# Optimization experiments

Hardware: AMD Instinct MI355X
Metric: run time of the kernel (lower is better)

Reference implementation:

```python
import jax, jax.numpy as jnp
import numpy as np

B, H, S, D = 2, 16, 2048, 64
DILATION_RATE = 2

def dilated_global_mask(seq_len: int, dilation_rate: int) -> jnp.ndarray:
    # mask[i, j] = 1 if |i - j| % dilation_rate == 0 else 0  -> [S, S] float32
    i = jnp.arange(seq_len)[:, None]
    j = jnp.arange(seq_len)[None, :]
    return ((jnp.abs(i - j) % dilation_rate) == 0).astype(jnp.float32)

def setup_inputs() -> dict:
    key = jax.random.key(0)
    kq, kk, kv = jax.random.split(key, 3)
    queries = jax.random.normal(kq, (B, H, S, D), dtype=jnp.float32)
    keys = jax.random.normal(kk, (B, H, S, D), dtype=jnp.float32)
    values = jax.random.normal(kv, (B, H, S, D), dtype=jnp.float32)
    return {"queries": queries, "keys": keys, "values": values}

def reference(queries, keys, values):
    depth = queries.shape[-1]
    # scores: [B, H, S, S]
    scores = jnp.einsum("bhqd,bhkd->bhqk", queries, keys)
    scores = scores / jnp.sqrt(jnp.asarray(depth, dtype=jnp.float32))
    gmask = dilated_global_mask(keys.shape[-2], DILATION_RATE)  # [S, S]
    # NOTE: multiplicative masking (masked scores become 0, not -inf), as in source
    masked_scores = scores * gmask
    attention_probs = jax.nn.softmax(masked_scores, axis=-1)
    # dropout is identity at inference (training=None)
    out = jnp.einsum("bhqk,bhkd->bhqd", attention_probs, values)
    return out
```

## Files before the change

kernel.cpp:

```cpp
#include <hip/hip_runtime.h>
#include <hip/hip_bf16.h>


#define B_   2
#define H_   16
#define S_   2048
#define D_   64
#define SP_  1024
#define BQ   128
#define FBQ  64
#define BK   64
#define NKT  (SP_ / BK)

#define QSCALE 0.180336884f

#if __has_builtin(__builtin_amdgcn_exp2f)
#define EXP2(x) __builtin_amdgcn_exp2f(x)
#else
#define EXP2(x) exp2f(x)
#endif

typedef __bf16 bf16x8 __attribute__((ext_vector_type(8)));
typedef __bf16 bf16x4 __attribute__((ext_vector_type(4)));
typedef float  f32x4  __attribute__((ext_vector_type(4)));
typedef short  s16x4  __attribute__((ext_vector_type(4)));

static __device__ __forceinline__ f32x4 mfma16(bf16x4 a, bf16x4 b, f32x4 c) {
    return __builtin_amdgcn_mfma_f32_16x16x16bf16_1k(
        __builtin_bit_cast(s16x4, a), __builtin_bit_cast(s16x4, b), c, 0, 0, 0);
}

#define KSW(r, c8) ((((c8) ^ ((r) & 7)) << 3))

__global__ __launch_bounds__(256) void conv2_kernel(const float* __restrict__ K,
                                                    const float* __restrict__ V,
                                                    __bf16* __restrict__ Kf,
                                                    __bf16* __restrict__ Vt,
                                                    __bf16* __restrict__ vsp) {
    const int id  = blockIdx.x;
    const int l2  = id >> 3;
    const int bh  = (id & 7) * 4 + (l2 & 3);
    const int kt  = l2 >> 2;
    const int tid = threadIdx.x;
    const float* Kb = K + (size_t)bh * S_ * D_;
    const float* Vb = V + (size_t)bh * S_ * D_;

    #pragma unroll
    for (int i = 0; i < 4; ++i) {
        const int u    = tid + 256 * i;
        const int par  = u >> 9;
        const int f    = (u >> 6) & 7;
        const int lane = u & 63;
        const int key  = kt * 64 + (f & 3) * 16 + (lane & 15);
        const int col  = ((f >> 2) * 4 + (lane >> 4)) * 8;
        const float* src = Kb + (size_t)(par + 2 * key) * D_ + col;
        const float4 a = *(const float4*)src;
        const float4 b = *(const float4*)(src + 4);
        bf16x8 w;
        w[0] = (__bf16)a.x; w[1] = (__bf16)a.y;
        w[2] = (__bf16)a.z; w[3] = (__bf16)a.w;
        w[4] = (__bf16)b.x; w[5] = (__bf16)b.y;
        w[6] = (__bf16)b.z; w[7] = (__bf16)b.w;
        const size_t bp = (size_t)(bh * 2 + par);
        *(bf16x8*)&Kf[((bp * NKT + kt) * 8 + f) * 512 + lane * 8] = w;
    }

    __shared__ __align__(16) __bf16 vt[64][80];
    const int row = tid >> 2;
    const int c0  = (tid & 3) * 16;

    #pragma unroll
    for (int par = 0; par < 2; ++par) {
        {
            const float* vsrc = Vb + (size_t)(par + 2 * (kt * 64 + row)) * D_ + c0;
            const float4 a0 = *(const float4*)(vsrc);
            const float4 a1 = *(const float4*)(vsrc + 4);
            const float4 a2 = *(const float4*)(vsrc + 8);
            const float4 a3 = *(const float4*)(vsrc + 12);
            bf16x8 w0, w1;
            w0[0] = (__bf16)a0.x; w0[1] = (__bf16)a0.y;
            w0[2] = (__bf16)a0.z; w0[3] = (__bf16)a0.w;
            w0[4] = (__bf16)a1.x; w0[5] = (__bf16)a1.y;
            w0[6] = (__bf16)a1.z; w0[7] = (__bf16)a1.w;
            w1[0] = (__bf16)a2.x; w1[1] = (__bf16)a2.y;
            w1[2] = (__bf16)a2.z; w1[3] = (__bf16)a2.w;
            w1[4] = (__bf16)a3.x; w1[5] = (__bf16)a3.y;
            w1[6] = (__bf16)a3.z; w1[7] = (__bf16)a3.w;
            *(bf16x8*)&vt[row][c0]     = w0;
            *(bf16x8*)&vt[row][c0 + 8] = w1;
        }
        __syncthreads();
        {
            const int d   = row;
            const int dt  = d >> 4;
            const int l15 = d & 15;
            const size_t bp = (size_t)(bh * 2 + par);
            const size_t tb = (bp * NKT + kt) * 16;
            float vsum = 0.f;
            #pragma unroll
            for (int cc2 = 0; cc2 < 2; ++cc2) {
                const int cc  = (tid & 3) * 2 + cc2;
                const int kt4 = cc >> 1;
                const int qa  = (cc & 1) * 2;
                bf16x4 wa, wb;
                #pragma unroll
                for (int m = 0; m < 4; ++m) {
                    const __bf16 x = vt[cc * 8 + m][d];
                    const __bf16 y = vt[cc * 8 + 4 + m][d];
                    wa[m] = x; wb[m] = y;
                    vsum += (float)x + (float)y;
                }
                const int g = kt4 * 4 + dt;
                *(bf16x4*)&Vt[(tb + g) * 256 + (qa * 16 + l15) * 4]       = wa;
                *(bf16x4*)&Vt[(tb + g) * 256 + ((qa + 1) * 16 + l15) * 4] = wb;
            }
            vsum += __shfl_down(vsum, 1);
            vsum += __shfl_down(vsum, 2);
            if ((tid & 3) == 0)
                vsp[(bp * NKT + kt) * 64 + d] = (__bf16)vsum;
        }
        __syncthreads();
    }
}

__global__ __launch_bounds__(256, 2) void attn6_kernel(const float* __restrict__ Q,
                                                       const __bf16* __restrict__ Kf,
                                                       const __bf16* __restrict__ Vt,
                                                       const __bf16* __restrict__ vsp,
                                                       float* __restrict__ out) {
    const int id  = blockIdx.x;
    const int l2  = id >> 3;
    const int bh  = (id & 7) * 4 + (l2 & 3);
    const int par = (l2 >> 2) & 1;
    const int qt  = l2 >> 3;
    const int bp  = bh * 2 + par;
    const int tid  = threadIdx.x;
    const int lane = tid & 63;
    const int wave = tid >> 6;
    const int l15  = lane & 15;
    const int quad = lane >> 4;

    __shared__ __align__(16) char arena[32768];

    const size_t base = (size_t)bh * S_ * D_;

    bf16x8 qf[2][2];
    #pragma unroll
    for (int qt2 = 0; qt2 < 2; ++qt2) {
        const int qrow = qt * BQ + wave * 32 + qt2 * 16 + l15;
        const float* qsrc = Q + base + (size_t)(par + 2 * qrow) * D_ + quad * 8;
        #pragma unroll
        for (int ks = 0; ks < 2; ++ks) {
            const float4 a = *(const float4*)(qsrc + ks * 32);
            const float4 b = *(const float4*)(qsrc + ks * 32 + 4);
            bf16x8 w;
            w[0] = (__bf16)(a.x * QSCALE); w[1] = (__bf16)(a.y * QSCALE);
            w[2] = (__bf16)(a.z * QSCALE); w[3] = (__bf16)(a.w * QSCALE);
            w[4] = (__bf16)(b.x * QSCALE); w[5] = (__bf16)(b.y * QSCALE);
            w[6] = (__bf16)(b.z * QSCALE); w[7] = (__bf16)(b.w * QSCALE);
            qf[qt2][ks] = w;
        }
    }

    const uint4* Kt4 = (const uint4*)(Kf + (size_t)bp * NKT * 4096);
    const uint4* Vt4 = (const uint4*)(Vt + (size_t)bp * NKT * 4096);
    uint4 sk0, sk1, sv0, sv1;

    auto issue_loads = [&](int kt) {
        const int o = kt * 512 + tid;
        sk0 = Kt4[o]; sk1 = Kt4[o + 256];
        sv0 = Vt4[o]; sv1 = Vt4[o + 256];
    };
    auto stage = [&](int buf) {
        uint4* kd = (uint4*)(arena + buf * 8192);
        uint4* vd = (uint4*)(arena + 16384 + buf * 8192);
        kd[tid] = sk0; kd[tid + 256] = sk1;
        vd[tid] = sv0; vd[tid + 256] = sv1;
    };

    issue_loads(0);
    stage(0);
    __syncthreads();

    f32x4 acc[2][4];
    #pragma unroll
    for (int q2 = 0; q2 < 2; ++q2)
        #pragma unroll
        for (int dt = 0; dt < 4; ++dt) acc[q2][dt] = (f32x4){0.f, 0.f, 0.f, 0.f};
    float l_acc[2] = {0.f, 0.f};

    for (int kt = 0; kt < NKT; ++kt) {
        const int cur = kt & 1;
        const bool pf = (kt + 1 < NKT);

        if (pf) issue_loads(kt + 1);

        const char* kb = arena + cur * 8192;
        const char* vb = arena + 16384 + cur * 8192;

        bf16x8 ka[2][4];
        #pragma unroll
        for (int ks = 0; ks < 2; ++ks)
            #pragma unroll
            for (int kt4 = 0; kt4 < 4; ++kt4)
                ka[ks][kt4] = *(const bf16x8*)(kb + (ks * 4 + kt4) * 1024 + lane * 16);
        bf16x4 va[4][4];
        #pragma unroll
        for (int kt4 = 0; kt4 < 4; ++kt4)
            #pragma unroll
            for (int dt = 0; dt < 4; ++dt)
                va[kt4][dt] = *(const bf16x4*)(vb + (kt4 * 4 + dt) * 512 + lane * 8);

        #pragma unroll
        for (int qt2 = 0; qt2 < 2; ++qt2) {
            f32x4 st[4];
            #pragma unroll
            for (int kt4 = 0; kt4 < 4; ++kt4) st[kt4] = (f32x4){0.f, 0.f, 0.f, 0.f};
            #pragma unroll
            for (int ks = 0; ks < 2; ++ks)
                #pragma unroll
                for (int kt4 = 0; kt4 < 4; ++kt4)
                    st[kt4] = __builtin_amdgcn_mfma_f32_16x16x32_bf16(
                        ka[ks][kt4], qf[qt2][ks], st[kt4], 0, 0, 0);
            #pragma unroll
            for (int kt4 = 0; kt4 < 4; ++kt4) {
                const float p0 = EXP2(st[kt4][0]);
                const float p1 = EXP2(st[kt4][1]);
                const float p2 = EXP2(st[kt4][2]);
                const float p3 = EXP2(st[kt4][3]);
                l_acc[qt2] += (p0 + p1) + (p2 + p3);
                bf16x4 pb;
                pb[0] = (__bf16)p0; pb[1] = (__bf16)p1;
                pb[2] = (__bf16)p2; pb[3] = (__bf16)p3;
                #pragma unroll
                for (int dt = 0; dt < 4; ++dt)
                    acc[qt2][dt] = mfma16(va[kt4][dt], pb, acc[qt2][dt]);
            }
        }

        if (pf) stage(1 - cur);
        __syncthreads();
    }

    float rz[2];
    #pragma unroll
    for (int qt2 = 0; qt2 < 2; ++qt2) {
        float Z = l_acc[qt2];
        Z += __shfl_xor(Z, 16);
        Z += __shfl_xor(Z, 32);
        rz[qt2] = 1.0f / (Z + 1024.0f);
    }
    const __bf16* vsb = vsp + (size_t)(bh * 2 + (1 - par)) * NKT * 64;
    f32x4 vs4[4];
    #pragma unroll
    for (int dt = 0; dt < 4; ++dt) {
        f32x4 s = (f32x4){0.f, 0.f, 0.f, 0.f};
        #pragma unroll
        for (int kt = 0; kt < NKT; ++kt) {
            const bf16x4 v = *(const bf16x4*)&vsb[kt * 64 + dt * 16 + quad * 4];
            s[0] += (float)v[0]; s[1] += (float)v[1];
            s[2] += (float)v[2]; s[3] += (float)v[3];
        }
        vs4[dt] = s;
    }

    float* tw = (float*)arena + wave * (16 * 68);
    #pragma unroll
    for (int qt2 = 0; qt2 < 2; ++qt2) {
        #pragma unroll
        for (int dt = 0; dt < 4; ++dt) {
            const f32x4 o = (acc[qt2][dt] + vs4[dt]) * rz[qt2];
            *(f32x4*)&tw[l15 * 68 + dt * 16 + quad * 4] = o;
        }
        #pragma unroll
        for (int i = 0; i < 4; ++i) {
            const int q = i * 4 + quad;
            const f32x4 ov = *(const f32x4*)&tw[q * 68 + l15 * 4];
            const int qg = par + 2 * (qt * BQ + wave * 32 + qt2 * 16 + q);
            *(f32x4*)&out[base + (size_t)qg * D_ + l15 * 4] = ov;
        }
    }
}

__global__ __launch_bounds__(1024) void vsum_kernel(const float* __restrict__ V,
                                                    float* __restrict__ vs) {
    const int bp  = blockIdx.x;
    const int bh  = bp >> 1;
    const int par = bp & 1;
    const int d   = threadIdx.x & 63;
    const int rg  = threadIdx.x >> 6;
    const float* Vb = V + (size_t)bh * S_ * D_;
    float s = 0.f;
    for (int r = rg; r < SP_; r += 16)
        s += Vb[(size_t)(par + 2 * r) * D_ + d];
    __shared__ float red[16][64];
    red[rg][d] = s;
    __syncthreads();
    if (rg == 0) {
        float t = 0.f;
        #pragma unroll
        for (int i = 0; i < 16; ++i) t += red[i][d];
        vs[(size_t)bp * 64 + d] = t;
    }
}

__global__ __launch_bounds__(256, 4) void attn_fb_kernel(const float* __restrict__ Q,
                                                         const float* __restrict__ K,
                                                         const float* __restrict__ V,
                                                         const float* __restrict__ vs,
                                                         float* __restrict__ out) {
    const int bh  = blockIdx.x;
    const int par = blockIdx.y;
    const int qt  = blockIdx.z;
    const int tid  = threadIdx.x;
    const int lane = tid & 63;
    const int wave = tid >> 6;
    const int l15  = lane & 15;
    const int quad = lane >> 4;

    __shared__ __align__(16) char arena[32768];
    __bf16 (*kbuf)[BK][64] = (__bf16 (*)[BK][64])arena;
    __bf16 (*vbuf)[D_][64] = (__bf16 (*)[D_][64])(arena + 16384);

    const size_t base = (size_t)bh * S_ * D_;
    const float* Qb = Q + base;
    const float* Kb = K + base;
    const float* Vb = V + base;

    bf16x8 qf[2];
    {
        const int qrow = qt * FBQ + wave * 16 + l15;
        const float* qsrc = Qb + (size_t)(par + 2 * qrow) * D_ + quad * 8;
        #pragma unroll
        for (int ks = 0; ks < 2; ++ks) {
            const float4 a = *(const float4*)(qsrc + ks * 32);
            const float4 b = *(const float4*)(qsrc + ks * 32 + 4);
            bf16x8 w;
            w[0] = (__bf16)(a.x * QSCALE); w[1] = (__bf16)(a.y * QSCALE);
            w[2] = (__bf16)(a.z * QSCALE); w[3] = (__bf16)(a.w * QSCALE);
            w[4] = (__bf16)(b.x * QSCALE); w[5] = (__bf16)(b.y * QSCALE);
            w[6] = (__bf16)(b.z * QSCALE); w[7] = (__bf16)(b.w * QSCALE);
            qf[ks] = w;
        }
    }

    const int kr0 = tid >> 3;
    const int kc8 = tid & 7;
    float4 pka[2], pkb[2];
    float  pv[16];

    auto issue_loads = [&](int kt) {
        #pragma unroll
        for (int i = 0; i < 2; ++i) {
            const int r = i * 32 + kr0;
            const float* ksrc = Kb + (size_t)(par + 2 * (kt * BK + r)) * D_ + kc8 * 8;
            pka[i] = *(const float4*)ksrc;
            pkb[i] = *(const float4*)(ksrc + 4);
        }
        #pragma unroll
        for (int i = 0; i < 2; ++i) {
            const int c = wave + 4 * i;
            const float* vsrc = Vb + (size_t)(par + 2 * (kt * BK + c * 8)) * D_ + lane;
            #pragma unroll
            for (int j = 0; j < 8; ++j)
                pv[i * 8 + j] = vsrc[(size_t)(2 * j) * D_];
        }
    };
    auto stage = [&](int buf) {
        #pragma unroll
        for (int i = 0; i < 2; ++i) {
            const int r = i * 32 + kr0;
            bf16x8 w;
            w[0] = (__bf16)pka[i].x; w[1] = (__bf16)pka[i].y;
            w[2] = (__bf16)pka[i].z; w[3] = (__bf16)pka[i].w;
            w[4] = (__bf16)pkb[i].x; w[5] = (__bf16)pkb[i].y;
            w[6] = (__bf16)pkb[i].z; w[7] = (__bf16)pkb[i].w;
            *(bf16x8*)&kbuf[buf][r][KSW(r, kc8)] = w;
        }
        #pragma unroll
        for (int i = 0; i < 2; ++i) {
            const int c = wave + 4 * i;
            bf16x8 w;
            #pragma unroll
            for (int j = 0; j < 8; ++j) w[j] = (__bf16)pv[i * 8 + j];
            *(bf16x8*)&vbuf[buf][lane][KSW(lane, c)] = w;
        }
    };

    issue_loads(0);
    stage(0);
    __syncthreads();

    f32x4 acc[4];
    #pragma unroll
    for (int dt = 0; dt < 4; ++dt) acc[dt] = (f32x4){0.f, 0.f, 0.f, 0.f};
    float l_acc = 0.f;

    for (int kt = 0; kt < NKT; ++kt) {
        const int cur = kt & 1;
        const bool pf = (kt + 1 < NKT);
        if (pf) issue_loads(kt + 1);

        const __bf16 (*kb)[64] = kbuf[cur];
        const __bf16 (*vb)[64] = vbuf[cur];

        bf16x8 ka[2][4];
        #pragma unroll
        for (int ks = 0; ks < 2; ++ks)
            #pragma unroll
            for (int kt4 = 0; kt4 < 4; ++kt4) {
                const int R = kt4 * 16 + l15;
                ka[ks][kt4] = *(const bf16x8*)&kb[R][KSW(R, ks * 4 + quad)];
            }
        bf16x4 va[4][4];
        #pragma unroll
        for (int dt = 0; dt < 4; ++dt) {
            const int R = dt * 16 + l15;
            const int ro = R & 7;
            #pragma unroll
            for (int kt4 = 0; kt4 < 4; ++kt4) {
                const int ch = (kt4 * 2 + (quad >> 1)) ^ ro;
                va[kt4][dt] = *(const bf16x4*)&vb[R][ch * 8 + (quad & 1) * 4];
            }
        }

        f32x4 st[4];
        #pragma unroll
        for (int kt4 = 0; kt4 < 4; ++kt4) st[kt4] = (f32x4){0.f, 0.f, 0.f, 0.f};
        #pragma unroll
        for (int ks = 0; ks < 2; ++ks)
            #pragma unroll
            for (int kt4 = 0; kt4 < 4; ++kt4)
                st[kt4] = __builtin_amdgcn_mfma_f32_16x16x32_bf16(
                    ka[ks][kt4], qf[ks], st[kt4], 0, 0, 0);
        #pragma unroll
        for (int kt4 = 0; kt4 < 4; ++kt4) {
            const float p0 = EXP2(st[kt4][0]);
            const float p1 = EXP2(st[kt4][1]);
            const float p2 = EXP2(st[kt4][2]);
            const float p3 = EXP2(st[kt4][3]);
            l_acc += (p0 + p1) + (p2 + p3);
            bf16x4 pb;
            pb[0] = (__bf16)p0; pb[1] = (__bf16)p1;
            pb[2] = (__bf16)p2; pb[3] = (__bf16)p3;
            #pragma unroll
            for (int dt = 0; dt < 4; ++dt)
                acc[dt] = mfma16(va[kt4][dt], pb, acc[dt]);
        }

        if (pf) stage(1 - cur);
        __syncthreads();
    }

    float Z = l_acc;
    Z += __shfl_xor(Z, 16);
    Z += __shfl_xor(Z, 32);
    const float rz = 1.0f / (Z + 1024.0f);
    const float* vso = vs + ((size_t)(bh * 2 + (1 - par))) * 64;

    float* tw = (float*)arena + wave * (16 * 68);
    #pragma unroll
    for (int dt = 0; dt < 4; ++dt) {
        const f32x4 vs4 = *(const f32x4*)&vso[dt * 16 + quad * 4];
        const f32x4 o = (acc[dt] + vs4) * rz;
        *(f32x4*)&tw[l15 * 68 + dt * 16 + quad * 4] = o;
    }
    #pragma unroll
    for (int i = 0; i < 4; ++i) {
        const int q = i * 4 + quad;
        const f32x4 ov = *(const f32x4*)&tw[q * 68 + l15 * 4];
        const int qg = par + 2 * (qt * FBQ + wave * 16 + q);
        *(f32x4*)&out[base + (size_t)qg * D_ + l15 * 4] = ov;
    }
}

extern "C" void kernel_launch(void* const* d_in, const int* in_sizes, int n_in,
                              void* d_out, int out_size, void* d_ws, size_t ws_size,
                              hipStream_t stream) {
    const float* Q = (const float*)d_in[0];
    const float* K = (const float*)d_in[1];
    const float* V = (const float*)d_in[2];
    float* out = (float*)d_out;

    const size_t KF_BYTES  = (size_t)64 * NKT * 4096 * sizeof(__bf16);
    const size_t VT_BYTES  = (size_t)64 * NKT * 4096 * sizeof(__bf16);
    const size_t VSP_BYTES = (size_t)64 * NKT * 64 * sizeof(__bf16);
    const size_t need = KF_BYTES + VT_BYTES + VSP_BYTES;

    if (ws_size >= need) {
        __bf16* Kf  = (__bf16*)d_ws;
        __bf16* Vt  = (__bf16*)((char*)d_ws + KF_BYTES);
        __bf16* vsp = (__bf16*)((char*)d_ws + KF_BYTES + VT_BYTES);
        conv2_kernel<<<dim3(512), dim3(256), 0, stream>>>(K, V, Kf, Vt, vsp);
        attn6_kernel<<<dim3(512), dim3(256), 0, stream>>>(Q, Kf, Vt, vsp, out);
    } else {
        float* vsn = (float*)d_ws;
        vsum_kernel<<<dim3(B_ * H_ * 2), dim3(1024), 0, stream>>>(V, vsn);
        attn_fb_kernel<<<dim3(B_ * H_, 2, SP_ / FBQ), dim3(256), 0, stream>>>(
            Q, K, V, vsn, out);
    }
}
```

Before: 121.2 us.

## Deepen K/V prefetch to two tiles ahead with barriers that skip vmcnt wait

The main attention loop now keeps two register sets of global K/V loads in flight, so loads are issued two tiles ahead. It also replaces __syncthreads with a custom barrier that waits only on LDS counters and leaves outstanding global loads pending. Together these aim to hide global-memory latency behind the MFMA work. The cost is higher register pressure at two blocks per CU, and correctness now depends on the compiler inserting vmcnt waits before the register values are staged.

```diff
diff --git a/kernel.cpp b/kernel.cpp
--- a/kernel.cpp
+++ b/kernel.cpp
@@ -31,6 +31,15 @@
 }
 
 #define KSW(r, c8) ((((c8) ^ ((r) & 7)) << 3))
+
+#define BARRIER_KEEP_VMCNT()                                   \
+    do {                                                       \
+        __builtin_amdgcn_sched_barrier(0);                     \
+        asm volatile("s_waitcnt lgkmcnt(0)" ::: "memory");     \
+        __builtin_amdgcn_sched_barrier(0);                     \
+        __builtin_amdgcn_s_barrier();                          \
+        __builtin_amdgcn_sched_barrier(0);                     \
+    } while (0)
 
 __global__ __launch_bounds__(256) void conv2_kernel(const float* __restrict__ K,
                                                     const float* __restrict__ V,
@@ -123,7 +132,7 @@
     }
 }
 
-__global__ __launch_bounds__(256, 2) void attn6_kernel(const float* __restrict__ Q,
+__global__ __launch_bounds__(256, 2) void attn7_kernel(const float* __restrict__ Q,
                                                        const __bf16* __restrict__ Kf,
                                                        const __bf16* __restrict__ Vt,
                                                        const __bf16* __restrict__ vsp,
@@ -164,23 +173,31 @@
 
     const uint4* Kt4 = (const uint4*)(Kf + (size_t)bp * NKT * 4096);
     const uint4* Vt4 = (const uint4*)(Vt + (size_t)bp * NKT * 4096);
-    uint4 sk0, sk1, sv0, sv1;
-
-    auto issue_loads = [&](int kt) {
+    uint4 skP0, skP1, svP0, svP1;
+    uint4 skQ0, skQ1, svQ0, svQ1;
+
+    auto issueP = [&](int kt) {
         const int o = kt * 512 + tid;
-        sk0 = Kt4[o]; sk1 = Kt4[o + 256];
-        sv0 = Vt4[o]; sv1 = Vt4[o + 256];
-    };
-    auto stage = [&](int buf) {
+        skP0 = Kt4[o]; skP1 = Kt4[o + 256];
+        svP0 = Vt4[o]; svP1 = Vt4[o + 256];
+    };
+    auto issueQ = [&](int kt) {
+        const int o = kt * 512 + tid;
+        skQ0 = Kt4[o]; skQ1 = Kt4[o + 256];
+        svQ0 = Vt4[o]; svQ1 = Vt4[o + 256];
+    };
+    auto stageP = [&](int buf) {
         uint4* kd = (uint4*)(arena + buf * 8192);
         uint4* vd = (uint4*)(arena + 16384 + buf * 8192);
-        kd[tid] = sk0; kd[tid + 256] = sk1;
-        vd[tid] = sv0; vd[tid + 256] = sv1;
-    };
-
-    issue_loads(0);
-    stage(0);
-    __syncthreads();
+        kd[tid] = skP0; kd[tid + 256] = skP1;
+        vd[tid] = svP0; vd[tid + 256] = svP1;
+    };
+    auto stageQ = [&](int buf) {
+        uint4* kd = (uint4*)(arena + buf * 8192);
+        uint4* vd = (uint4*)(arena + 16384 + buf * 8192);
+        kd[tid] = skQ0; kd[tid + 256] = skQ1;
+        vd[tid] = svQ0; vd[tid + 256] = svQ1;
+    };
 
     f32x4 acc[2][4];
     #pragma unroll
@@ -189,15 +206,7 @@
         for (int dt = 0; dt < 4; ++dt) acc[q2][dt] = (f32x4){0.f, 0.f, 0.f, 0.f};
     float l_acc[2] = {0.f, 0.f};
 
-    for (int kt = 0; kt < NKT; ++kt) {
-        const int cur = kt & 1;
-        const bool pf = (kt + 1 < NKT);
-
-        if (pf) issue_loads(kt + 1);
-
-        const char* kb = arena + cur * 8192;
-        const char* vb = arena + 16384 + cur * 8192;
-
+    auto compute = [&](const char* kb, const char* vb) {
         bf16x8 ka[2][4];
         #pragma unroll
         for (int ks = 0; ks < 2; ++ks)
@@ -237,9 +246,27 @@
                     acc[qt2][dt] = mfma16(va[kt4][dt], pb, acc[qt2][dt]);
             }
         }
-
-        if (pf) stage(1 - cur);
-        __syncthreads();
+    };
+
+    const char* kb0 = arena;
+    const char* kb1 = arena + 8192;
+    const char* vb0 = arena + 16384;
+    const char* vb1 = arena + 24576;
+
+    issueP(0);
+    stageP(0);
+    issueQ(1);
+    BARRIER_KEEP_VMCNT();
+
+    for (int t = 0; t < NKT; t += 2) {
+        if (t + 2 < NKT) issueP(t + 2);
+        compute(kb0, vb0);
+        stageQ(1);
+        BARRIER_KEEP_VMCNT();
+        if (t + 3 < NKT) issueQ(t + 3);
+        compute(kb1, vb1);
+        if (t + 2 < NKT) stageP(0);
+        BARRIER_KEEP_VMCNT();
     }
 
     float rz[2];
@@ -492,7 +519,7 @@
         __bf16* Vt  = (__bf16*)((char*)d_ws + KF_BYTES);
         __bf16* vsp = (__bf16*)((char*)d_ws + KF_BYTES + VT_BYTES);
         conv2_kernel<<<dim3(512), dim3(256), 0, stream>>>(K, V, Kf, Vt, vsp);
-        attn6_kernel<<<dim3(512), dim3(256), 0, stream>>>(Q, Kf, Vt, vsp, out);
+        attn7_kernel<<<dim3(512), dim3(256), 0, stream>>>(Q, Kf, Vt, vsp, out);
     } else {
         float* vsn = (float*)d_ws;
         vsum_kernel<<<dim3(B_ * H_ * 2), dim3(1024), 0, stream>>>(V, vsn);
```

Result: no change. 122.2 us (+0.8%).
